# Optimization experiments

Hardware: AMD Instinct MI355X
Metric: run time of the kernel (lower is better)

Reference implementation:

```python
import jax, jax.numpy as jnp
import numpy as np

B, D, E, H, F, V = 65536, 8, 16, 80, 9, 100000
IN = E * (F + 1)  # 160


def setup_inputs() -> dict:
    key = jax.random.key(0)
    ks = jax.random.split(key, 14)
    pid = jax.random.randint(ks[0], (B,), 0, D + 1)            # 0 = padding, 1..D = domains
    feats = jax.random.randint(ks[1], (B, F), 0, V)
    emb_pid = (jax.random.normal(ks[2], (D + 1, E), jnp.float32) * 0.1).at[0].set(0.0)
    emb_feats = (jax.random.normal(ks[3], (F, V + 1, E), jnp.float32) * 0.1).at[:, 0, :].set(0.0)
    shared_w1 = jax.random.normal(ks[4], (IN, H), jnp.float32) * 0.1
    dom_w1 = jax.random.normal(ks[5], (D, IN, H), jnp.float32) * 0.1
    shared_b1 = jax.random.normal(ks[6], (H,), jnp.float32) * 0.1
    dom_b1 = jax.random.normal(ks[7], (D, H), jnp.float32) * 0.1
    shared_w2 = jax.random.normal(ks[8], (H,), jnp.float32) * 0.1
    dom_w2 = jax.random.normal(ks[9], (D, H), jnp.float32) * 0.1
    shared_b2 = jax.random.normal(ks[10], (), jnp.float32) * 0.1
    dom_b2 = jax.random.normal(ks[11], (D,), jnp.float32) * 0.1
    dl_w = jax.random.normal(ks[12], (E,), jnp.float32) * 0.1
    dl_b = jax.random.normal(ks[13], (), jnp.float32) * 0.1
    return {"pid": pid, "feats": feats, "emb_pid": emb_pid, "emb_feats": emb_feats,
            "shared_w1": shared_w1, "dom_w1": dom_w1, "shared_b1": shared_b1, "dom_b1": dom_b1,
            "shared_w2": shared_w2, "dom_w2": dom_w2, "shared_b2": shared_b2, "dom_b2": dom_b2,
            "dl_w": dl_w, "dl_b": dl_b}


def reference(pid, feats, emb_pid, emb_feats, shared_w1, dom_w1, shared_b1, dom_b1,
              shared_w2, dom_w2, shared_b2, dom_b2, dl_w, dl_b):
    # embedding lookup + relu (dropout is identity at inference)
    e_pid = jax.nn.relu(emb_pid[pid])                          # (B, E)
    e_f = jax.nn.relu(emb_feats[jnp.arange(F), feats])         # (B, F, E)
    out = jnp.concatenate([e_pid, e_f.reshape(B, F * E)], axis=-1)  # (B, IN)
    # star-merge: elementwise product of shared and per-domain kernels, additive biases
    W1 = shared_w1[None] * dom_w1                              # (D, IN, H)
    b1 = shared_b1[None] + dom_b1                              # (D, H)
    h = jax.nn.relu(jnp.einsum('bi,dih->dbh', out, W1) + b1[:, None, :])  # (D, B, H)
    W2 = shared_w2[None] * dom_w2                              # (D, H)
    b2 = shared_b2 + dom_b2                                    # (D,)
    l = jnp.einsum('dbh,dh->db', h, W2) + b2[:, None]          # (D, B)
    # scatter-combine: each sample takes its own domain's logit (0 for padding pid)
    sel = pid[None, :] == (jnp.arange(D) + 1)[:, None]         # (D, B)
    logits = jnp.sum(jnp.where(sel, l, 0.0), axis=0)           # (B,)
    domain_logits = e_pid @ dl_w + dl_b                        # (B,)
    return logits + domain_logits
```

## Files before the change

### kernel.cpp

```cpp
#include <hip/hip_runtime.h>
#include <hip/hip_bf16.h>

#define NB 65536
#define ND 8
#define NE 16
#define NH 80
#define NF 9
#define NV 100000
#define NIN 160
#define WND 1024
#define NWND (NB / WND)

typedef __attribute__((ext_vector_type(8))) short short8;
typedef __attribute__((ext_vector_type(4))) float float4v;

__device__ inline unsigned short f2bf(float x) {
  unsigned int u = __float_as_uint(x);
  return (unsigned short)((u + 0x7fffu + ((u >> 16) & 1u)) >> 16);
}
__device__ inline unsigned int cvt2(float x, float y) {
  union { __hip_bfloat162 h; unsigned int u; } cv;
  cv.h = __float22bfloat162_rn(make_float2(x, y));
  return cv.u;
}

__global__ __launch_bounds__(512, 4) void k_main(
    const int* __restrict__ pid, const int* __restrict__ feats,
    const float* __restrict__ emb_pid, const float* __restrict__ emb_feats,
    const float* __restrict__ sw1, const float* __restrict__ dw1,
    const float* __restrict__ sb1, const float* __restrict__ db1,
    const float* __restrict__ sw2, const float* __restrict__ dw2,
    const float* __restrict__ sb2, const float* __restrict__ db2,
    const float* __restrict__ dl_w, const float* __restrict__ dl_b,
    float* __restrict__ out) {
  const int d = blockIdx.x >> 6;
  const int wnd = blockIdx.x & 63;
  const int t = threadIdx.x, wave = t >> 6, lane = t & 63;

  __shared__ unsigned short sA[2][64][168];
  __shared__ unsigned short sBF[5][5][4][16][8];
  __shared__ int sOrig[WND];
  __shared__ int cnt0[8], cnt1[8];

  const int b0 = wnd * WND + t;
  const int b1 = b0 + 512;
  const int p0 = pid[b0];
  const int p1 = pid[b1];

  for (int i = t; i < NIN * NH; i += 512) {
    int k = i / NH, n = i % NH;
    float w = sw1[i] * dw1[d * (NIN * NH) + i];
    sBF[n >> 4][k >> 5][(k >> 3) & 3][n & 15][k & 7] = f2bf(w);
  }

  const float dlb = dl_b[0];
  float dlacc = dlb;
  unsigned int ep[8];
  {
    const float* __restrict__ row = emb_pid + (d + 1) * NE;
#pragma unroll
    for (int i = 0; i < NE; i += 2) {
      float x0 = fmaxf(row[i], 0.f), x1 = fmaxf(row[i + 1], 0.f);
      dlacc = fmaf(x0, dl_w[i], dlacc);
      dlacc = fmaf(x1, dl_w[i + 1], dlacc);
      ep[i >> 1] = cvt2(x0, x1);
    }
  }
  float b1l[5], w2l[5];
#pragma unroll
  for (int nt = 0; nt < 5; ++nt) {
    int h = nt * 16 + (lane & 15);
    b1l[nt] = sb1[h] + db1[d * NH + h];
    w2l[nt] = sw2[h] * dw2[d * NH + h];
  }
  const float b2 = sb2[0] + db2[d];

  if (d == 0) {
    if (p0 == 0) out[b0] = dlb;
    if (p1 == 0) out[b1] = dlb;
  }

  unsigned long long m0 = __ballot(p0 == d + 1);
  unsigned long long m1 = __ballot(p1 == d + 1);
  if (lane == 0) { cnt0[wave] = (int)__popcll(m0); cnt1[wave] = (int)__popcll(m1); }
  const unsigned long long lt = (1ull << lane) - 1ull;
  const int r0 = (int)__popcll(m0 & lt);
  const int r1 = (int)__popcll(m1 & lt);
  __syncthreads();
  int base0 = 0, tot0 = 0, base1 = 0;
#pragma unroll
  for (int w = 0; w < 8; ++w) {
    if (w < wave) { base0 += cnt0[w]; base1 += cnt1[w]; }
    tot0 += cnt0[w];
  }
  int c = tot0;
#pragma unroll
  for (int w = 0; w < 8; ++w) c += cnt1[w];
  if (p0 == d + 1) sOrig[base0 + r0] = b0;
  if (p1 == d + 1) sOrig[tot0 + base1 + r1] = b1;
  __syncthreads();

  if (c == 0) return;
  const int ntiles = (c + 63) >> 6;
  const bool prod = wave >= 4;

  auto stage = [&](int buf, int g0) {
    const int s = (t & 255) >> 2, q = t & 3;
    int ss = g0 + s; if (ss >= c) ss = c - 1;
    const int bb = sOrig[ss];
    int idx[NF];
#pragma unroll
    for (int f = 0; f < NF; ++f) idx[f] = feats[bb * NF + f];
    float4 vv[NF];
#pragma unroll
    for (int f = 0; f < NF; ++f)
      vv[f] = *(const float4*)(emb_feats +
                               (size_t)((f * (NV + 1) + idx[f]) * NE + q * 4));
    if (q < 2) {
      unsigned int* dst = (unsigned int*)&sA[buf][s][0];
#pragma unroll
      for (int j = 0; j < 4; ++j) dst[q * 4 + j] = ep[q * 4 + j];
    }
#pragma unroll
    for (int f = 0; f < NF; ++f) {
      unsigned int lo = cvt2(fmaxf(vv[f].x, 0.f), fmaxf(vv[f].y, 0.f));
      unsigned int hi = cvt2(fmaxf(vv[f].z, 0.f), fmaxf(vv[f].w, 0.f));
      unsigned int* dst = (unsigned int*)&sA[buf][s][16 + f * 16];
      dst[q * 2] = lo;
      dst[q * 2 + 1] = hi;
    }
  };

  if (prod) stage(0, 0);
  __syncthreads();

  for (int k = 0; k < ntiles; ++k) {
    const int g0 = k * 64;
    if (prod) {
      if (k + 1 < ntiles) stage((k + 1) & 1, g0 + 64);
    } else if (g0 + wave * 16 < c) {
      const int buf = k & 1;
      float4v acc[5];
#pragma unroll
      for (int nt = 0; nt < 5; ++nt)
        acc[nt] = (float4v){b1l[nt], b1l[nt], b1l[nt], b1l[nt]};
      const int arow = wave * 16 + (lane & 15);
      const int koff = (lane >> 4) * 8;
#pragma unroll
      for (int ks = 0; ks < 5; ++ks) {
        short8 af = *(const short8*)&sA[buf][arow][ks * 32 + koff];
#pragma unroll
        for (int nt = 0; nt < 5; ++nt) {
          short8 bf = *(const short8*)&sBF[nt][ks][lane >> 4][lane & 15][0];
          acc[nt] = __builtin_amdgcn_mfma_f32_16x16x32_bf16(af, bf, acc[nt], 0, 0, 0);
        }
      }
      float pr[4];
#pragma unroll
      for (int r = 0; r < 4; ++r) {
        float a2 = 0.f;
#pragma unroll
        for (int nt = 0; nt < 5; ++nt) a2 = fmaf(fmaxf(acc[nt][r], 0.f), w2l[nt], a2);
        pr[r] = a2;
      }
#pragma unroll
      for (int r = 0; r < 4; ++r) {
        pr[r] += __shfl_xor(pr[r], 1);
        pr[r] += __shfl_xor(pr[r], 2);
        pr[r] += __shfl_xor(pr[r], 4);
        pr[r] += __shfl_xor(pr[r], 8);
      }
      if ((lane & 15) == 0) {
        int srow2 = wave * 16 + (lane >> 4) * 4;
#pragma unroll
        for (int r = 0; r < 4; ++r) {
          int kk = g0 + srow2 + r;
          if (kk < c) out[sOrig[kk]] = pr[r] + b2 + dlacc;
        }
      }
    }
    __syncthreads();
  }
}

extern "C" void kernel_launch(void* const* d_in, const int* in_sizes, int n_in,
                              void* d_out, int out_size, void* d_ws, size_t ws_size,
                              hipStream_t stream) {
  const int*   pid      = (const int*)d_in[0];
  const int*   feats    = (const int*)d_in[1];
  const float* emb_pid  = (const float*)d_in[2];
  const float* emb_f    = (const float*)d_in[3];
  const float* sw1      = (const float*)d_in[4];
  const float* dw1      = (const float*)d_in[5];
  const float* sb1      = (const float*)d_in[6];
  const float* db1      = (const float*)d_in[7];
  const float* sw2      = (const float*)d_in[8];
  const float* dw2      = (const float*)d_in[9];
  const float* sb2      = (const float*)d_in[10];
  const float* db2      = (const float*)d_in[11];
  const float* dl_w     = (const float*)d_in[12];
  const float* dl_b     = (const float*)d_in[13];
  float* out = (float*)d_out;
  (void)d_ws; (void)ws_size;

  k_main<<<NWND * ND, 512, 0, stream>>>(pid, feats, emb_pid, emb_f, sw1, dw1,
                                        sb1, db1, sw2, dw2, sb2, db2, dl_w,
                                        dl_b, out);
}
```

Measured before the change: 24.60 us.

## Double window size, add triple-buffered staging, and coalesce feature index loads

Each block now handles 2048 samples per domain instead of 1024, which halves the grid and amortises the per-block cost of building the merged weight tile. The stage buffer becomes triple-buffered so producers can run two tiles ahead, and the first two tiles are prefetched by both wave groups. Feature indices are loaded cooperatively across each four-lane group and broadcast with shuffles, and LDS stores are widened to uint2. The trade-off is fewer blocks (256) and a lower occupancy hint, which may reduce latency hiding on the gather-bound path.

```diff
diff --git a/kernel.cpp b/kernel.cpp
--- a/kernel.cpp
+++ b/kernel.cpp
@@ -8,7 +8,7 @@
 #define NF 9
 #define NV 100000
 #define NIN 160
-#define WND 1024
+#define WND 2048
 #define NWND (NB / WND)
 
 typedef __attribute__((ext_vector_type(8))) short short8;
@@ -24,7 +24,7 @@
   return cv.u;
 }
 
-__global__ __launch_bounds__(512, 4) void k_main(
+__global__ __launch_bounds__(512, 2) void k_main(
     const int* __restrict__ pid, const int* __restrict__ feats,
     const float* __restrict__ emb_pid, const float* __restrict__ emb_feats,
     const float* __restrict__ sw1, const float* __restrict__ dw1,
@@ -33,19 +33,19 @@
     const float* __restrict__ sb2, const float* __restrict__ db2,
     const float* __restrict__ dl_w, const float* __restrict__ dl_b,
     float* __restrict__ out) {
-  const int d = blockIdx.x >> 6;
-  const int wnd = blockIdx.x & 63;
+  const int d = blockIdx.x >> 5;
+  const int wnd = blockIdx.x & 31;
   const int t = threadIdx.x, wave = t >> 6, lane = t & 63;
 
-  __shared__ unsigned short sA[2][64][168];
+  __shared__ unsigned short sA[3][64][168];
   __shared__ unsigned short sBF[5][5][4][16][8];
   __shared__ int sOrig[WND];
-  __shared__ int cnt0[8], cnt1[8];
-
-  const int b0 = wnd * WND + t;
-  const int b1 = b0 + 512;
-  const int p0 = pid[b0];
-  const int p1 = pid[b1];
+  __shared__ int scnt[4][8];
+
+  const int bbase = wnd * WND + t;
+  int pp[4];
+#pragma unroll
+  for (int pass = 0; pass < 4; ++pass) pp[pass] = pid[bbase + pass * 512];
 
   for (int i = t; i < NIN * NH; i += 512) {
     int k = i / NH, n = i % NH;
@@ -76,41 +76,57 @@
   const float b2 = sb2[0] + db2[d];
 
   if (d == 0) {
-    if (p0 == 0) out[b0] = dlb;
-    if (p1 == 0) out[b1] = dlb;
-  }
-
-  unsigned long long m0 = __ballot(p0 == d + 1);
-  unsigned long long m1 = __ballot(p1 == d + 1);
-  if (lane == 0) { cnt0[wave] = (int)__popcll(m0); cnt1[wave] = (int)__popcll(m1); }
+#pragma unroll
+    for (int pass = 0; pass < 4; ++pass)
+      if (pp[pass] == 0) out[bbase + pass * 512] = dlb;
+  }
+
   const unsigned long long lt = (1ull << lane) - 1ull;
-  const int r0 = (int)__popcll(m0 & lt);
-  const int r1 = (int)__popcll(m1 & lt);
+  int rr[4];
+#pragma unroll
+  for (int pass = 0; pass < 4; ++pass) {
+    unsigned long long m = __ballot(pp[pass] == d + 1);
+    if (lane == 0) scnt[pass][wave] = (int)__popcll(m);
+    rr[pass] = (int)__popcll(m & lt);
+  }
   __syncthreads();
-  int base0 = 0, tot0 = 0, base1 = 0;
-#pragma unroll
-  for (int w = 0; w < 8; ++w) {
-    if (w < wave) { base0 += cnt0[w]; base1 += cnt1[w]; }
-    tot0 += cnt0[w];
-  }
-  int c = tot0;
-#pragma unroll
-  for (int w = 0; w < 8; ++w) c += cnt1[w];
-  if (p0 == d + 1) sOrig[base0 + r0] = b0;
-  if (p1 == d + 1) sOrig[tot0 + base1 + r1] = b1;
+  int pbase[4], run = 0;
+#pragma unroll
+  for (int pass = 0; pass < 4; ++pass) {
+    int bw = 0, tt = 0;
+#pragma unroll
+    for (int w = 0; w < 8; ++w) {
+      int v = scnt[pass][w];
+      if (w < wave) bw += v;
+      tt += v;
+    }
+    pbase[pass] = run + bw;
+    run += tt;
+  }
+  const int c = run;
+#pragma unroll
+  for (int pass = 0; pass < 4; ++pass)
+    if (pp[pass] == d + 1) sOrig[pbase[pass] + rr[pass]] = bbase + pass * 512;
   __syncthreads();
 
   if (c == 0) return;
   const int ntiles = (c + 63) >> 6;
-  const bool prod = wave >= 4;
-
-  auto stage = [&](int buf, int g0) {
-    const int s = (t & 255) >> 2, q = t & 3;
+
+  auto stage = [&](int buf, int g0, int t256) {
+    const int s = t256 >> 2, q = t256 & 3;
     int ss = g0 + s; if (ss >= c) ss = c - 1;
     const int bb = sOrig[ss];
+    const int fb = bb * NF;
+    int ia = feats[fb + q];
+    int ib = feats[fb + 4 + q];
+    int ic = (q == 0) ? feats[fb + 8] : 0;
+    const int gl = lane & ~3;
     int idx[NF];
 #pragma unroll
-    for (int f = 0; f < NF; ++f) idx[f] = feats[bb * NF + f];
+    for (int f = 0; f < 4; ++f) idx[f] = __shfl(ia, gl + f);
+#pragma unroll
+    for (int f = 0; f < 4; ++f) idx[4 + f] = __shfl(ib, gl + f);
+    idx[8] = __shfl(ic, gl);
     float4 vv[NF];
 #pragma unroll
     for (int f = 0; f < NF; ++f)
@@ -123,59 +139,61 @@
     }
 #pragma unroll
     for (int f = 0; f < NF; ++f) {
-      unsigned int lo = cvt2(fmaxf(vv[f].x, 0.f), fmaxf(vv[f].y, 0.f));
-      unsigned int hi = cvt2(fmaxf(vv[f].z, 0.f), fmaxf(vv[f].w, 0.f));
-      unsigned int* dst = (unsigned int*)&sA[buf][s][16 + f * 16];
-      dst[q * 2] = lo;
-      dst[q * 2 + 1] = hi;
+      uint2 w;
+      w.x = cvt2(fmaxf(vv[f].x, 0.f), fmaxf(vv[f].y, 0.f));
+      w.y = cvt2(fmaxf(vv[f].z, 0.f), fmaxf(vv[f].w, 0.f));
+      *(uint2*)((unsigned int*)&sA[buf][s][16 + f * 16] + q * 2) = w;
     }
   };
 
-  if (prod) stage(0, 0);
+  if (wave < 4) stage(0, 0, t);
+  else if (ntiles > 1) stage(1, 64, t - 256);
   __syncthreads();
 
   for (int k = 0; k < ntiles; ++k) {
-    const int g0 = k * 64;
-    if (prod) {
-      if (k + 1 < ntiles) stage((k + 1) & 1, g0 + 64);
-    } else if (g0 + wave * 16 < c) {
-      const int buf = k & 1;
-      float4v acc[5];
-#pragma unroll
-      for (int nt = 0; nt < 5; ++nt)
-        acc[nt] = (float4v){b1l[nt], b1l[nt], b1l[nt], b1l[nt]};
-      const int arow = wave * 16 + (lane & 15);
-      const int koff = (lane >> 4) * 8;
-#pragma unroll
-      for (int ks = 0; ks < 5; ++ks) {
-        short8 af = *(const short8*)&sA[buf][arow][ks * 32 + koff];
-#pragma unroll
-        for (int nt = 0; nt < 5; ++nt) {
-          short8 bf = *(const short8*)&sBF[nt][ks][lane >> 4][lane & 15][0];
-          acc[nt] = __builtin_amdgcn_mfma_f32_16x16x32_bf16(af, bf, acc[nt], 0, 0, 0);
-        }
-      }
-      float pr[4];
-#pragma unroll
-      for (int r = 0; r < 4; ++r) {
-        float a2 = 0.f;
-#pragma unroll
-        for (int nt = 0; nt < 5; ++nt) a2 = fmaf(fmaxf(acc[nt][r], 0.f), w2l[nt], a2);
-        pr[r] = a2;
-      }
-#pragma unroll
-      for (int r = 0; r < 4; ++r) {
-        pr[r] += __shfl_xor(pr[r], 1);
-        pr[r] += __shfl_xor(pr[r], 2);
-        pr[r] += __shfl_xor(pr[r], 4);
-        pr[r] += __shfl_xor(pr[r], 8);
-      }
-      if ((lane & 15) == 0) {
-        int srow2 = wave * 16 + (lane >> 4) * 4;
+    if (wave >= 4) {
+      if (k + 2 < ntiles) stage((k + 2) % 3, (k + 2) * 64, t - 256);
+    } else {
+      const int g0 = k * 64;
+      if (g0 + wave * 16 < c) {
+        const int buf = k % 3;
+        float4v acc[5];
+#pragma unroll
+        for (int nt = 0; nt < 5; ++nt)
+          acc[nt] = (float4v){b1l[nt], b1l[nt], b1l[nt], b1l[nt]};
+        const int arow = wave * 16 + (lane & 15);
+        const int koff = (lane >> 4) * 8;
+#pragma unroll
+        for (int ks = 0; ks < 5; ++ks) {
+          short8 af = *(const short8*)&sA[buf][arow][ks * 32 + koff];
+#pragma unroll
+          for (int nt = 0; nt < 5; ++nt) {
+            short8 bf = *(const short8*)&sBF[nt][ks][lane >> 4][lane & 15][0];
+            acc[nt] = __builtin_amdgcn_mfma_f32_16x16x32_bf16(af, bf, acc[nt], 0, 0, 0);
+          }
+        }
+        float pr[4];
 #pragma unroll
         for (int r = 0; r < 4; ++r) {
-          int kk = g0 + srow2 + r;
-          if (kk < c) out[sOrig[kk]] = pr[r] + b2 + dlacc;
+          float a2 = 0.f;
+#pragma unroll
+          for (int nt = 0; nt < 5; ++nt) a2 = fmaf(fmaxf(acc[nt][r], 0.f), w2l[nt], a2);
+          pr[r] = a2;
+        }
+#pragma unroll
+        for (int r = 0; r < 4; ++r) {
+          pr[r] += __shfl_xor(pr[r], 1);
+          pr[r] += __shfl_xor(pr[r], 2);
+          pr[r] += __shfl_xor(pr[r], 4);
+          pr[r] += __shfl_xor(pr[r], 8);
+        }
+        if ((lane & 15) == 0) {
+          int srow2 = wave * 16 + (lane >> 4) * 4;
+#pragma unroll
+          for (int r = 0; r < 4; ++r) {
+            int kk = g0 + srow2 + r;
+            if (kk < c) out[sOrig[kk]] = pr[r] + b2 + dlacc;
+          }
         }
       }
     }
```

Result: no change. 24.32 us (-1.1%).
